# Kernel optimization log

Hardware: AMD Instinct MI355X
Metric: run time of the kernel (lower is better)

Reference implementation:

```python
import math
import jax, jax.numpy as jnp
import numpy as np

B, LA, LB, H = 16, 1024, 1024, 512
NEG = -10000000.0


def setup_inputs() -> dict:
    key = jax.random.key(0)
    k1, k2, k3, k4 = jax.random.split(key, 4)
    a = jax.random.normal(k1, (B, LA, H), dtype=jnp.float32)
    b = jax.random.normal(k2, (B, LB, H), dtype=jnp.float32)
    mask_a = jax.random.randint(k3, (B, LA, 1), 0, 2, dtype=jnp.int32)
    mask_b = jax.random.randint(k4, (B, LB, 1), 0, 2, dtype=jnp.int32)
    temperature = jnp.asarray(1.0 / math.sqrt(H), dtype=jnp.float32)
    return {"a": a, "b": b, "mask_a": mask_a, "mask_b": mask_b, "temperature": temperature}


def reference(a, b, mask_a, mask_b, temperature):
    # attn[b,i,j] = <a_i, b_j> * temperature  -> [B, LA, LB]
    attn = jnp.einsum("bid,bjd->bij", a, b) * temperature
    # pairwise validity mask: outer product of per-token masks
    mask = jnp.einsum("bik,bjk->bij", mask_a.astype(jnp.float32), mask_b.astype(jnp.float32)) > 0
    attn = jnp.where(mask, attn, NEG)
    attn_a = jax.nn.softmax(attn, axis=1)  # softmax over a-tokens
    attn_b = jax.nn.softmax(attn, axis=2)  # softmax over b-tokens
    feature_b = jnp.einsum("bij,bid->bjd", attn_a, a)  # [B, LB, H]
    feature_a = jnp.einsum("bij,bjd->bid", attn_b, b)  # [B, LA, H]
    return (feature_a, feature_b)
```

## Files before the change

kernel.cpp:

```cpp
#include <hip/hip_runtime.h>
#include <hip/hip_bf16.h>

#define NB_ 16
#define LA_ 1024
#define LB_ 1024
#define H_  512

typedef __attribute__((ext_vector_type(8))) short short8;
typedef __attribute__((ext_vector_type(4))) float f32x4;

using bf16 = __hip_bfloat16;

__device__ __forceinline__ float bf2f(unsigned short u) {
    union { unsigned int i; float f; } c; c.i = ((unsigned)u) << 16; return c.f;
}
__device__ __forceinline__ unsigned short f2bf(float f) {
    bf16 h = __float2bfloat16(f);
    return *(unsigned short*)&h;
}

__device__ __forceinline__ void load_lds16(const void* g, void* l) {
    __builtin_amdgcn_global_load_lds(
        (const __attribute__((address_space(1))) void*)g,
        (__attribute__((address_space(3))) void*)l, 16, 0, 0);
}

__device__ __forceinline__ void gemm_core64(
    const unsigned short* __restrict__ A, const unsigned short* __restrict__ B,
    int lda, int ldb, int K,
    unsigned short* ldsA, unsigned short* ldsB, f32x4 acc[4][4])
{
    const int t = threadIdx.x;
    const int wave = t >> 6, lane = t & 63;
    const int wr = wave >> 1, wc = wave & 1;
    const int lm = lane & 15, q = lane >> 4;

    int aoff[4], boff[4];
#pragma unroll
    for (int f = 0; f < 4; f++) {
        const int ra = wr * 64 + f * 16 + lm;
        aoff[f] = ra * 128 + ((q ^ (ra & 7)) << 4);
        const int rb = wc * 64 + f * 16 + lm;
        boff[f] = rb * 128 + ((q ^ (rb & 7)) << 4);
    }

    const int row0 = wave * 8 + (lane >> 3);
    const int sc = (lane & 7) ^ (row0 & 7);
    const unsigned short* gA0 = A + (size_t)row0 * lda + sc * 8;
    const unsigned short* gB0 = B + (size_t)row0 * ldb + sc * 8;
    const int sA = 32 * lda, sB = 32 * ldb;
    char* lA = (char*)ldsA + wave * 1024;
    char* lB = (char*)ldsB + wave * 1024;

    for (int k0 = 0; k0 < K; k0 += 64) {
        __syncthreads();
#pragma unroll
        for (int s = 0; s < 4; s++) {
            load_lds16(gA0 + k0 + s * sA, lA + s * 4096);
            load_lds16(gB0 + k0 + s * sB, lB + s * 4096);
        }
        __syncthreads();
#pragma unroll
        for (int kk = 0; kk < 2; kk++) {
            const int kx = kk << 6;
            short8 av[4];
#pragma unroll
            for (int fm = 0; fm < 4; fm++)
                av[fm] = *(const short8*)((const char*)ldsA + (aoff[fm] ^ kx));
#pragma unroll
            for (int fn = 0; fn < 4; fn++) {
                const short8 bv = *(const short8*)((const char*)ldsB + (boff[fn] ^ kx));
#pragma unroll
                for (int fm = 0; fm < 4; fm++)
                    acc[fm][fn] = __builtin_amdgcn_mfma_f32_16x16x32_bf16(
                        av[fm], bv, acc[fm][fn], 0, 0, 0);
            }
        }
    }
}

__global__ __launch_bounds__(256) void k_gemm_attn(
    const unsigned short* __restrict__ a_bf, const unsigned short* __restrict__ b_bf,
    const int* __restrict__ mask_a, const int* __restrict__ mask_b,
    const float* __restrict__ temp_p,
    unsigned short* __restrict__ E, unsigned short* __restrict__ ET,
    float* __restrict__ l_row, float* __restrict__ l_col)
{
    __shared__ unsigned short lds[16384];
    unsigned short* ldsA = lds;
    unsigned short* ldsB = lds + 8192;

    const int g = blockIdx.x;
    const int batch = g & 15;
    const int qq = g >> 4;
    const int i0 = (qq >> 3) * 128, j0 = (qq & 7) * 128;

    const unsigned short* A = a_bf + (size_t)batch * LA_ * H_ + (size_t)i0 * H_;
    const unsigned short* B = b_bf + (size_t)batch * LB_ * H_ + (size_t)j0 * H_;
    f32x4 acc[4][4];
#pragma unroll
    for (int x = 0; x < 4; x++)
#pragma unroll
        for (int y = 0; y < 4; y++) acc[x][y] = 0;

    gemm_core64(A, B, H_, H_, H_, ldsA, ldsB, acc);

    const float temp = temp_p[0];
    const int t = threadIdx.x, wave = t >> 6, lane = t & 63;
    const int wr = wave >> 1, wc = wave & 1, lm = lane & 15, q = lane >> 4;
    const int* map = mask_a + batch * LA_;
    const int* mbp = mask_b + batch * LB_;
    unsigned short* Ep  = E  + (size_t)batch * LA_ * LB_;
    unsigned short* ETp = ET + (size_t)batch * LB_ * LA_;
    float* lrp = l_row + batch * LA_;
    float* lcp = l_col + batch * LB_;

    int mb[4];
#pragma unroll
    for (int fn = 0; fn < 4; fn++) mb[fn] = mbp[j0 + wc * 64 + fn * 16 + lm];

#pragma unroll
    for (int fm = 0; fm < 4; fm++) {
        const int ib = i0 + wr * 64 + fm * 16 + q * 4;
        int ma[4];
#pragma unroll
        for (int r = 0; r < 4; r++) ma[r] = map[ib + r];
#pragma unroll
        for (int fn = 0; fn < 4; fn++) {
            const int j = j0 + wc * 64 + fn * 16 + lm;
            ushort4 pk;
            unsigned short* pp = (unsigned short*)&pk;
#pragma unroll
            for (int r = 0; r < 4; r++) {
                const float e = (ma[r] && mb[fn]) ? __expf(acc[fm][fn][r] * temp) : 0.0f;
                acc[fm][fn][r] = e;
                pp[r] = f2bf(e);
            }
            *(ushort4*)(ETp + (size_t)j * LA_ + ib) = pk;
        }
    }

#pragma unroll
    for (int fm = 0; fm < 4; fm++)
#pragma unroll
        for (int r = 0; r < 4; r++) {
            float s = acc[fm][0][r] + acc[fm][1][r] + acc[fm][2][r] + acc[fm][3][r];
            s += __shfl_xor(s, 1, 16); s += __shfl_xor(s, 2, 16);
            s += __shfl_xor(s, 4, 16); s += __shfl_xor(s, 8, 16);
            if (lm == 0) atomicAdd(&lrp[i0 + wr * 64 + fm * 16 + q * 4 + r], s);
        }
#pragma unroll
    for (int fn = 0; fn < 4; fn++) {
        float s = 0.0f;
#pragma unroll
        for (int fm = 0; fm < 4; fm++)
#pragma unroll
            for (int r = 0; r < 4; r++) s += acc[fm][fn][r];
        s += __shfl_xor(s, 16, 64); s += __shfl_xor(s, 32, 64);
        if (lane < 16) atomicAdd(&lcp[j0 + wc * 64 + fn * 16 + lm], s);
    }

    __syncthreads();
#pragma unroll
    for (int fm = 0; fm < 4; fm++)
#pragma unroll
        for (int fn = 0; fn < 4; fn++)
#pragma unroll
            for (int r = 0; r < 4; r++) {
                const int il = wr * 64 + fm * 16 + q * 4 + r;
                const int jl = wc * 64 + fn * 16 + lm;
                lds[il * 128 + (((jl >> 3) ^ ((il >> 1) & 7)) << 3) + (jl & 7)] =
                    f2bf(acc[fm][fn][r]);
            }
    __syncthreads();
#pragma unroll
    for (int rep = 0; rep < 8; rep++) {
        const int il = (t >> 4) + rep * 16;
        const int jc = t & 15;
        const int phys = jc ^ ((il >> 1) & 7);
        short8 v = *(const short8*)(lds + il * 128 + phys * 8);
        *(short8*)(Ep + (size_t)(i0 + il) * LB_ + j0 + jc * 8) = v;
    }
}

__global__ __launch_bounds__(256) void k_gemm_feat(
    const unsigned short* __restrict__ E, const unsigned short* __restrict__ ET,
    const unsigned short* __restrict__ aT, const unsigned short* __restrict__ bT,
    const int* __restrict__ mask_a, const int* __restrict__ mask_b,
    const int* __restrict__ nA, const int* __restrict__ nB,
    const float* __restrict__ l_row, const float* __restrict__ l_col,
    const float* __restrict__ mean_a, const float* __restrict__ mean_b,
    float* __restrict__ out)
{
    __shared__ unsigned short lds[16384];
    unsigned short* ldsA = lds;
    unsigned short* ldsB = lds + 8192;

    const int g = blockIdx.x;
    const int zc = g & 31;
    const int qq = g >> 5;
    const int n0 = (qq & 3) * 128, m0 = (qq >> 2) * 128;

    const int batch = zc & 15;
    const bool isA = zc < 16;
    const unsigned short* Amat = (isA ? E : ET) + (size_t)batch * 1024 * 1024;
    const unsigned short* Bm   = (isA ? bT : aT) + (size_t)batch * H_ * 1024;
    const int* mp   = (isA ? mask_a : mask_b) + batch * 1024;
    const int nn    = (isA ? nB : nA)[batch];
    const float* sp = (isA ? l_row : l_col) + batch * 1024;
    const float* mv = (isA ? mean_b : mean_a) + batch * H_;
    float* op = out + (isA ? (size_t)0 : (size_t)NB_ * LA_ * H_) + (size_t)batch * 1024 * H_;

    f32x4 acc[4][4];
#pragma unroll
    for (int x = 0; x < 4; x++)
#pragma unroll
        for (int y = 0; y < 4; y++) acc[x][y] = 0;

    gemm_core64(Amat + (size_t)m0 * 1024, Bm + (size_t)n0 * 1024,
                1024, 1024, 1024, ldsA, ldsB, acc);

    const int t = threadIdx.x, wave = t >> 6, lane = t & 63;
    const int wr = wave >> 1, wc = wave & 1, lm = lane & 15, q = lane >> 4;

    float mval[4];
#pragma unroll
    for (int fn = 0; fn < 4; fn++) mval[fn] = mv[n0 + wc * 64 + fn * 16 + lm];

#pragma unroll
    for (int fm = 0; fm < 4; fm++) {
        const int ib = m0 + wr * 64 + fm * 16 + q * 4;
#pragma unroll
        for (int r = 0; r < 4; r++) {
            const int i = ib + r;
            const bool valid = (mp[i] != 0) && (nn > 0);
            const float inv = valid ? 1.0f / sp[i] : 0.0f;
#pragma unroll
            for (int fn = 0; fn < 4; fn++) {
                const int d = n0 + wc * 64 + fn * 16 + lm;
                op[(size_t)i * H_ + d] = valid ? acc[fm][fn][r] * inv : mval[fn];
            }
        }
    }
}

__global__ __launch_bounds__(256) void k_prep(
    const float* __restrict__ a, const float* __restrict__ b,
    unsigned short* __restrict__ aN, unsigned short* __restrict__ bN,
    unsigned short* __restrict__ aT, unsigned short* __restrict__ bT,
    float* __restrict__ mean_a, float* __restrict__ mean_b)
{
    __shared__ unsigned short lds[64][68];
    __shared__ float smean[64];
    const int z = blockIdx.z;
    const int batch = z & 15, sel = z >> 4;
    const float* src = sel ? b : a;
    unsigned short* np = (sel ? bN : aN) + (size_t)batch * 1024 * H_;
    unsigned short* tp = (sel ? bT : aT) + (size_t)batch * H_ * 1024;
    float* mdst = (sel ? mean_b : mean_a) + batch * H_;
    const float* sp = src + (size_t)batch * 1024 * H_;

    const int d0 = blockIdx.x * 64, i0 = blockIdx.y * 64;
    const int t = threadIdx.x;
    if (t < 64) smean[t] = 0.0f;
    const int c4 = (t & 15) * 4;
#pragma unroll
    for (int it = 0; it < 4; it++) {
        const int r = (t >> 4) + it * 16;
        float4 v = *(const float4*)(sp + (size_t)(i0 + r) * H_ + d0 + c4);
        ushort4 u = make_ushort4(f2bf(v.x), f2bf(v.y), f2bf(v.z), f2bf(v.w));
        *(ushort4*)(np + (size_t)(i0 + r) * H_ + d0 + c4) = u;
        *(ushort4*)&lds[r][c4] = u;
    }
    __syncthreads();
#pragma unroll
    for (int it = 0; it < 4; it++) {
        const int dd = (t >> 4) + it * 16;
        const int i4 = (t & 15) * 4;
        ushort4 u = make_ushort4(lds[i4][dd], lds[i4 + 1][dd], lds[i4 + 2][dd], lds[i4 + 3][dd]);
        *(ushort4*)(tp + (size_t)(d0 + dd) * 1024 + i0 + i4) = u;
        atomicAdd(&smean[dd], bf2f(u.x) + bf2f(u.y) + bf2f(u.z) + bf2f(u.w));
    }
    __syncthreads();
    if (t < 64) atomicAdd(&mdst[d0 + t], smean[t] * (1.0f / 1024.0f));
}

__global__ __launch_bounds__(256) void k_init(
    float* __restrict__ accum_zero,
    const int* __restrict__ mask_a, const int* __restrict__ mask_b,
    int* __restrict__ nA, int* __restrict__ nB)
{
    const int g = blockIdx.x, t = threadIdx.x;
    if (g < 48) {
        *(float4*)(accum_zero + (size_t)(g * 256 + t) * 4) = make_float4(0, 0, 0, 0);
        return;
    }
    const int sel = g - 48;
    const int batch = sel & 15, which = sel >> 4;
    const int* m = (which ? mask_b : mask_a) + batch * 1024;
    int s = m[t] + m[t + 256] + m[t + 512] + m[t + 768];
    __shared__ int red[256];
    red[t] = s;
    __syncthreads();
    for (int off = 128; off; off >>= 1) {
        if (t < off) red[t] += red[t + off];
        __syncthreads();
    }
    if (t == 0) (which ? nB : nA)[batch] = red[0];
}

extern "C" void kernel_launch(void* const* d_in, const int* in_sizes, int n_in,
                              void* d_out, int out_size, void* d_ws, size_t ws_size,
                              hipStream_t stream)
{
    const float* a      = (const float*)d_in[0];
    const float* b      = (const float*)d_in[1];
    const int*   mask_a = (const int*)d_in[2];
    const int*   mask_b = (const int*)d_in[3];
    const float* temp   = (const float*)d_in[4];
    float* out = (float*)d_out;

    char* ws = (char*)d_ws;
    size_t off = 0;
    unsigned short* E    = (unsigned short*)(ws + off); off += (size_t)NB_ * LA_ * LB_ * 2;
    unsigned short* ET   = (unsigned short*)(ws + off); off += (size_t)NB_ * LB_ * LA_ * 2;
    unsigned short* a_bf = (unsigned short*)(ws + off); off += (size_t)NB_ * LA_ * H_ * 2;
    unsigned short* b_bf = (unsigned short*)(ws + off); off += (size_t)NB_ * LB_ * H_ * 2;
    unsigned short* aT   = (unsigned short*)(ws + off); off += (size_t)NB_ * H_ * LA_ * 2;
    unsigned short* bT   = (unsigned short*)(ws + off); off += (size_t)NB_ * H_ * LB_ * 2;
    float* l_row  = (float*)(ws + off); off += (size_t)NB_ * LA_ * 4;
    float* l_col  = (float*)(ws + off); off += (size_t)NB_ * LB_ * 4;
    float* mean_a = (float*)(ws + off); off += (size_t)NB_ * H_ * 4;
    float* mean_b = (float*)(ws + off); off += (size_t)NB_ * H_ * 4;
    int*   nA     = (int*)(ws + off); off += 64;
    int*   nB     = (int*)(ws + off); off += 64;

    k_init<<<dim3(80), 256, 0, stream>>>(l_row, mask_a, mask_b, nA, nB);

    k_prep<<<dim3(H_ / 64, 1024 / 64, 32), 256, 0, stream>>>(
        a, b, a_bf, b_bf, aT, bT, mean_a, mean_b);

    k_gemm_attn<<<dim3(1024), 256, 0, stream>>>(
        a_bf, b_bf, mask_a, mask_b, temp, E, ET, l_row, l_col);

    k_gemm_feat<<<dim3(1024), 256, 0, stream>>>(
        E, ET, aT, bT, mask_a, mask_b, nA, nB, l_row, l_col, mean_a, mean_b, out);
}
```

Baseline: 227.3 us.

## Replace direct-to-LDS GEMM core with register-prefetched double-buffered K=32 pipeline

```diff
diff --git a/kernel.cpp b/kernel.cpp
--- a/kernel.cpp
+++ b/kernel.cpp
@@ -19,16 +19,10 @@
     return *(unsigned short*)&h;
 }
 
-__device__ __forceinline__ void load_lds16(const void* g, void* l) {
-    __builtin_amdgcn_global_load_lds(
-        (const __attribute__((address_space(1))) void*)g,
-        (__attribute__((address_space(3))) void*)l, 16, 0, 0);
-}
-
-__device__ __forceinline__ void gemm_core64(
+__device__ __forceinline__ void gemm_pipe32(
     const unsigned short* __restrict__ A, const unsigned short* __restrict__ B,
     int lda, int ldb, int K,
-    unsigned short* ldsA, unsigned short* ldsB, f32x4 acc[4][4])
+    unsigned short* lds, f32x4 acc[4][4])
 {
     const int t = threadIdx.x;
     const int wave = t >> 6, lane = t & 63;
@@ -39,42 +33,87 @@
 #pragma unroll
     for (int f = 0; f < 4; f++) {
         const int ra = wr * 64 + f * 16 + lm;
-        aoff[f] = ra * 128 + ((q ^ (ra & 7)) << 4);
+        aoff[f] = ra * 64 + ((q ^ ((ra >> 1) & 3)) << 4);
         const int rb = wc * 64 + f * 16 + lm;
-        boff[f] = rb * 128 + ((q ^ (rb & 7)) << 4);
-    }
-
-    const int row0 = wave * 8 + (lane >> 3);
-    const int sc = (lane & 7) ^ (row0 & 7);
-    const unsigned short* gA0 = A + (size_t)row0 * lda + sc * 8;
-    const unsigned short* gB0 = B + (size_t)row0 * ldb + sc * 8;
-    const int sA = 32 * lda, sB = 32 * ldb;
-    char* lA = (char*)ldsA + wave * 1024;
-    char* lB = (char*)ldsB + wave * 1024;
-
-    for (int k0 = 0; k0 < K; k0 += 64) {
-        __syncthreads();
-#pragma unroll
-        for (int s = 0; s < 4; s++) {
-            load_lds16(gA0 + k0 + s * sA, lA + s * 4096);
-            load_lds16(gB0 + k0 + s * sB, lB + s * 4096);
-        }
-        __syncthreads();
-#pragma unroll
-        for (int kk = 0; kk < 2; kk++) {
-            const int kx = kk << 6;
+        boff[f] = rb * 64 + ((q ^ ((rb >> 1) & 3)) << 4) + 8192;
+    }
+
+    const int r0 = t >> 2, c = t & 3;
+    const int r1 = r0 + 64;
+    const unsigned short* gA0 = A + (size_t)r0 * lda + c * 8;
+    const unsigned short* gA1 = A + (size_t)r1 * lda + c * 8;
+    const unsigned short* gB0 = B + (size_t)r0 * ldb + c * 8;
+    const unsigned short* gB1 = B + (size_t)r1 * ldb + c * 8;
+    const int pA0 = r0 * 64 + ((c ^ ((r0 >> 1) & 3)) << 4);
+    const int pA1 = r1 * 64 + ((c ^ ((r1 >> 1) & 3)) << 4);
+    const int pB0 = 8192 + pA0;
+    const int pB1 = 8192 + pA1;
+
+    uint4 vA0[2], vA1[2], vB0[2], vB1[2];
+    vA0[0] = *(const uint4*)gA0;        vA1[0] = *(const uint4*)gA1;
+    vB0[0] = *(const uint4*)gB0;        vB1[0] = *(const uint4*)gB1;
+    vA0[1] = *(const uint4*)(gA0 + 32); vA1[1] = *(const uint4*)(gA1 + 32);
+    vB0[1] = *(const uint4*)(gB0 + 32); vB1[1] = *(const uint4*)(gB1 + 32);
+
+    {
+        char* sb = (char*)lds;
+        *(uint4*)(sb + pA0) = vA0[0]; *(uint4*)(sb + pA1) = vA1[0];
+        *(uint4*)(sb + pB0) = vB0[0]; *(uint4*)(sb + pB1) = vB1[0];
+    }
+    asm volatile("s_waitcnt lgkmcnt(0)\n\ts_barrier" ::: "memory");
+
+    const int T = K >> 5;
+    for (int k = 0; k < T; k += 2) {
+        {
+            if (k + 2 < T) {
+                const int o = (k + 2) * 32;
+                vA0[0] = *(const uint4*)(gA0 + o); vA1[0] = *(const uint4*)(gA1 + o);
+                vB0[0] = *(const uint4*)(gB0 + o); vB1[0] = *(const uint4*)(gB1 + o);
+            }
+            const char* base = (const char*)lds;
             short8 av[4];
 #pragma unroll
-            for (int fm = 0; fm < 4; fm++)
-                av[fm] = *(const short8*)((const char*)ldsA + (aoff[fm] ^ kx));
+            for (int fm = 0; fm < 4; fm++) av[fm] = *(const short8*)(base + aoff[fm]);
+            {
+                char* sb = (char*)lds + 16384;
+                *(uint4*)(sb + pA0) = vA0[1]; *(uint4*)(sb + pA1) = vA1[1];
+                *(uint4*)(sb + pB0) = vB0[1]; *(uint4*)(sb + pB1) = vB1[1];
+            }
 #pragma unroll
             for (int fn = 0; fn < 4; fn++) {
-                const short8 bv = *(const short8*)((const char*)ldsB + (boff[fn] ^ kx));
+                const short8 bv = *(const short8*)(base + boff[fn]);
 #pragma unroll
                 for (int fm = 0; fm < 4; fm++)
                     acc[fm][fn] = __builtin_amdgcn_mfma_f32_16x16x32_bf16(
                         av[fm], bv, acc[fm][fn], 0, 0, 0);
             }
+            asm volatile("s_waitcnt lgkmcnt(0)\n\ts_barrier" ::: "memory");
+        }
+        {
+            const int k1 = k + 1;
+            if (k1 + 2 < T) {
+                const int o = (k1 + 2) * 32;
+                vA0[1] = *(const uint4*)(gA0 + o); vA1[1] = *(const uint4*)(gA1 + o);
+                vB0[1] = *(const uint4*)(gB0 + o); vB1[1] = *(const uint4*)(gB1 + o);
+            }
+            const char* base = (const char*)lds + 16384;
+            short8 av[4];
+#pragma unroll
+            for (int fm = 0; fm < 4; fm++) av[fm] = *(const short8*)(base + aoff[fm]);
+            if (k1 + 1 < T) {
+                char* sb = (char*)lds;
+                *(uint4*)(sb + pA0) = vA0[0]; *(uint4*)(sb + pA1) = vA1[0];
+                *(uint4*)(sb + pB0) = vB0[0]; *(uint4*)(sb + pB1) = vB1[0];
+            }
+#pragma unroll
+            for (int fn = 0; fn < 4; fn++) {
+                const short8 bv = *(const short8*)(base + boff[fn]);
+#pragma unroll
+                for (int fm = 0; fm < 4; fm++)
+                    acc[fm][fn] = __builtin_amdgcn_mfma_f32_16x16x32_bf16(
+                        av[fm], bv, acc[fm][fn], 0, 0, 0);
+            }
+            asm volatile("s_waitcnt lgkmcnt(0)\n\ts_barrier" ::: "memory");
         }
     }
 }
@@ -87,8 +126,6 @@
     float* __restrict__ l_row, float* __restrict__ l_col)
 {
     __shared__ unsigned short lds[16384];
-    unsigned short* ldsA = lds;
-    unsigned short* ldsB = lds + 8192;
 
     const int g = blockIdx.x;
     const int batch = g & 15;
@@ -103,7 +140,7 @@
 #pragma unroll
         for (int y = 0; y < 4; y++) acc[x][y] = 0;
 
-    gemm_core64(A, B, H_, H_, H_, ldsA, ldsB, acc);
+    gemm_pipe32(A, B, H_, H_, H_, lds, acc);
 
     const float temp = temp_p[0];
     const int t = threadIdx.x, wave = t >> 6, lane = t & 63;
@@ -193,8 +230,6 @@
     float* __restrict__ out)
 {
     __shared__ unsigned short lds[16384];
-    unsigned short* ldsA = lds;
-    unsigned short* ldsB = lds + 8192;
 
     const int g = blockIdx.x;
     const int zc = g & 31;
@@ -217,8 +252,8 @@
 #pragma unroll
         for (int y = 0; y < 4; y++) acc[x][y] = 0;
 
-    gemm_core64(Amat + (size_t)m0 * 1024, Bm + (size_t)n0 * 1024,
-                1024, 1024, 1024, ldsA, ldsB, acc);
+    gemm_pipe32(Amat + (size_t)m0 * 1024, Bm + (size_t)n0 * 1024,
+                1024, 1024, 1024, lds, acc);
 
     const int t = threadIdx.x, wave = t >> 6, lane = t & 63;
     const int wr = wave >> 1, wc = wave & 1, lm = lane & 15, q = lane >> 4;
```

New measurement: 403.1 us. 77.4% more time.
